# Kernel optimization log

Measured on AMD Instinct MI355X. Metric: run time of the kernel, lower is better.

## Reference

```python
import jax, jax.numpy as jnp
import numpy as np

B, C, H, W = 2, 192, 64, 64
NHEADS = 8


def setup_inputs() -> dict:
    key = jax.random.key(0)
    ks = jax.random.split(key, 6)
    L = H * W
    return {
        "x": jax.random.normal(ks[0], (B, C, H, W), dtype=jnp.float32),
        "mask": jax.random.normal(ks[1], (B, L, L), dtype=jnp.float32),
        "w_qkv": jax.random.normal(ks[2], (3 * C, C), dtype=jnp.float32) * (1.0 / np.sqrt(C)),
        "b_qkv": jax.random.normal(ks[3], (3 * C,), dtype=jnp.float32) * 0.02,
        "w_proj": jax.random.normal(ks[4], (C, C), dtype=jnp.float32) * (1.0 / np.sqrt(C)),
        "b_proj": jax.random.normal(ks[5], (C,), dtype=jnp.float32) * 0.02,
        "num_heads": NHEADS,
    }


def reference(x, mask, w_qkv, b_qkv, w_proj, b_proj, num_heads):
    b, c, h, w = x.shape
    L = h * w
    hd = c // num_heads  # head dim
    # 1x1 conv == per-pixel linear over channels
    qkv = jnp.einsum('bchw,oc->bohw', x, w_qkv) + b_qkv[None, :, None, None]
    q, k, v = jnp.split(qkv, 3, axis=1)  # each [b, c, h, w]

    def to_heads(t):
        # b (head hd) h w -> b head (h w) hd
        return t.reshape(b, num_heads, hd, L).transpose(0, 1, 3, 2)

    q, k, v = to_heads(q), to_heads(k), to_heads(v)
    scale = num_heads ** (-0.5)  # NOTE: original scales by num_heads, not head_dim
    attn = jnp.einsum('bnld,bnmd->bnlm', q, k) * scale + mask[:, None, :, :]
    attn = jax.nn.softmax(attn, axis=-1)
    out = jnp.einsum('bnlm,bnmd->bnld', attn, v)  # [b, head, L, hd]
    # b head L hd -> b (head hd) h w
    out = out.transpose(0, 1, 3, 2).reshape(b, c, h, w)
    out = jnp.einsum('bchw,oc->bohw', out, w_proj) + b_proj[None, :, None, None]
    return out
```

## Files before the change

kernel.cpp:

```cpp
#include <hip/hip_runtime.h>

#define B_  2
#define C_  192
#define L_  4096
#define NH_ 8
#define HD_ 24
#define C3_ 576
#define KV_ 64
#define NSPL_ 4
#define LSPL_ (L_ / NSPL_)
#define NTS_ (LSPL_ / KV_)
#define HG_ 4

typedef _Float16 f16;
typedef __attribute__((ext_vector_type(8))) f16 f16x8;
typedef __attribute__((ext_vector_type(16))) float f32x16;

#define L2E_ 1.4426950408889634f

__device__ __forceinline__ int pk2(float a, float b) {
    union { __fp16 h __attribute__((ext_vector_type(2))); int i; } u;
    u.h = __builtin_amdgcn_cvt_pkrtz(a, b);
    return u.i;
}
__device__ __forceinline__ int pk2_rte(float a, float b) {
    union { f16 h[2]; int i; } u;
    u.h[0] = (f16)a; u.h[1] = (f16)b;
    return u.i;
}
__device__ __forceinline__ float ex2(float x) {
    float r;
    asm("v_exp_f32 %0, %1" : "=v"(r) : "v"(x));
    return r;
}
__device__ __forceinline__ float lg2(float x) {
    float r;
    asm("v_log_f32 %0, %1" : "=v"(r) : "v"(x));
    return r;
}

union Frag { f16x8 v; int i[4]; };

#define MFMA32(A, Bx, Cc) __builtin_amdgcn_mfma_f32_32x32x16_f16((A), (Bx), (Cc), 0, 0, 0)

__device__ __forceinline__ void gload4(const void* g, void* lds) {
    typedef const unsigned int __attribute__((address_space(1))) as1u;
    typedef unsigned int __attribute__((address_space(3))) as3u;
    __builtin_amdgcn_global_load_lds((as1u*)g,
                                     (as3u*)(unsigned int)(unsigned long long)lds,
                                     4, 0, 0);
}
__device__ __forceinline__ void gload16(const void* g, void* lds) {
    typedef const unsigned int __attribute__((address_space(1))) as1u;
    typedef unsigned int __attribute__((address_space(3))) as3u;
    __builtin_amdgcn_global_load_lds((as1u*)g,
                                     (as3u*)(unsigned int)(unsigned long long)lds,
                                     16, 0, 0);
}

__global__ __launch_bounds__(256) void lin_qkv(const float* __restrict__ a,
                                               const float* __restrict__ w,
                                               const float* __restrict__ bias,
                                               unsigned int* __restrict__ q2,
                                               unsigned int* __restrict__ k2,
                                               unsigned short* __restrict__ v16) {
    __shared__ float wl[8][C_];
    const int og  = blockIdx.x;
    const int b   = blockIdx.y >> 4;
    const int lt  = blockIdx.y & 15;
    const int tid = threadIdx.x;

    for (int e = tid; e < 8 * C_; e += 256) wl[e / C_][e % C_] = w[og * 8 * C_ + e];
    __syncthreads();

    const int l = lt * 256 + tid;
    float acc[8];
#pragma unroll
    for (int j = 0; j < 8; ++j) acc[j] = bias[og * 8 + j];

    const float* ap = a + (size_t)b * C_ * L_ + l;
#pragma unroll 2
    for (int c = 0; c < C_; ++c) {
        const float xv = ap[(size_t)c * L_];
#pragma unroll
        for (int j = 0; j < 8; ++j) acc[j] = fmaf(wl[j][c], xv, acc[j]);
    }

    const float qscale = 0.35355339059327373f * L2E_;
    if (og < 48) {
        unsigned int* dst = (og < 24) ? q2 : k2;
        const int og_ = (og < 24) ? og : og - 24;
        const float sc = (og < 24) ? qscale : 1.f;
        const int h = og_ / 3, j0 = (og_ % 3) * 4;
        unsigned int* p = dst + ((size_t)(b * NH_ + h) * 12 + j0) * L_ + l;
#pragma unroll
        for (int j = 0; j < 4; ++j)
            p[(size_t)j * L_] = pk2_rte(acc[2 * j] * sc, acc[2 * j + 1] * sc);
    } else {
        const int og_ = og - 48;
        const int h = og_ / 3, d0 = (og_ % 3) * 8;
        unsigned short* p = v16 + ((size_t)(b * NH_ + h) * 24 + d0) * L_ + l;
#pragma unroll
        for (int j = 0; j < 8; ++j) {
            union { f16 hf; unsigned short us; } cv;
            cv.hf = (f16)acc[j];
            p[(size_t)j * L_] = cv.us;
        }
    }
}

__global__ __launch_bounds__(256) void lin_kernel(const float* __restrict__ a,
                                                  const float* __restrict__ w,
                                                  const float* __restrict__ bias,
                                                  float* __restrict__ out, int OC) {
    __shared__ float wl[8][C_];
    const int og  = blockIdx.x;
    const int b   = blockIdx.y >> 4;
    const int lt  = blockIdx.y & 15;
    const int tid = threadIdx.x;

    for (int e = tid; e < 8 * C_; e += 256) wl[e / C_][e % C_] = w[og * 8 * C_ + e];
    __syncthreads();

    const int l = lt * 256 + tid;
    float acc[8];
#pragma unroll
    for (int j = 0; j < 8; ++j) acc[j] = bias[og * 8 + j];

    const float* ap = a + (size_t)b * C_ * L_ + l;
#pragma unroll 2
    for (int c = 0; c < C_; ++c) {
        const float xv = ap[(size_t)c * L_];
#pragma unroll
        for (int j = 0; j < 8; ++j) acc[j] = fmaf(wl[j][c], xv, acc[j]);
    }

    float* op = out + ((size_t)b * OC + og * 8) * L_ + l;
#pragma unroll
    for (int j = 0; j < 8; ++j) op[(size_t)j * L_] = acc[j];
}

__global__ __launch_bounds__(256) void attn_mfma(const unsigned int* __restrict__ q2,
                                                 const unsigned int* __restrict__ k2,
                                                 const unsigned short* __restrict__ v16,
                                                 const float* __restrict__ mask,
                                                 unsigned short* __restrict__ po,
                                                 float* __restrict__ pms) {
    const int tid  = threadIdx.x;
    const int lane = tid & 63;
    const int wid  = tid >> 6;
    const int hi   = lane >> 5;
    const int lq   = lane & 31;
    const int bid  = blockIdx.x;
    const int qt   = bid & 31;
    const int r    = bid >> 5;
    const int b    = r & 1;
    const int hg   = (r >> 1) & 1;
    const int sp   = r >> 2;
    const int qrow = qt * 128 + wid * 32 + lq;
    const int kv0  = sp * LSPL_;
    const int hbase = hg * HG_;

    __shared__ int k_lds[2][HG_][16][64];
    __shared__ int v_lds[2][HG_][32][32];

#pragma unroll
    for (int z = 0; z < 8; ++z) {
        const int wd = z * 256 + tid;
        k_lds[wd >> 10][(wd >> 8) & 3][12 + ((wd >> 6) & 3)][wd & 63] = 0;
    }

    const unsigned int*   qb   = q2  + (size_t)(b * NH_ + hbase) * 12 * L_;
    const unsigned int*   kb_w = k2  + (size_t)(b * NH_ + hbase + wid) * 12 * L_;
    const unsigned short* vb_w = v16 + (size_t)(b * NH_ + hbase + wid) * 24 * L_;
    const float* mrow = mask + ((size_t)b * L_ + qrow) * L_;

    int bq[HG_][8];
#pragma unroll
    for (int H = 0; H < HG_; ++H)
#pragma unroll
        for (int s = 0; s < 2; ++s)
#pragma unroll
            for (int t = 0; t < 4; ++t) {
                const int dpq = 8 * s + 4 * hi + t;
                bq[H][s * 4 + t] = (dpq < 12) ? qb[(size_t)(H * 12 + dpq) * L_ + qrow] : 0;
            }

#define STAGE(BF, KK) do {                                                    \
    _Pragma("unroll")                                                         \
    for (int j_ = 0; j_ < 3; ++j_) {                                          \
        const int dp_ = j_ * 4 + (lane >> 4);                                 \
        gload16(kb_w + (size_t)dp_ * L_ + (KK) + 4 * (lane & 15),             \
                &k_lds[BF][wid][0][0] + j_ * 256);                            \
    }                                                                         \
    _Pragma("unroll")                                                         \
    for (int j_ = 0; j_ < 12; ++j_) {                                         \
        const int e_ = j_ * 64 + lane;                                        \
        const int d_ = e_ >> 5, sl_ = e_ & 31;                                \
        gload4(vb_w + (size_t)d_ * L_ + (KK) + 2 * (sl_ ^ d_),                \
               &v_lds[BF][wid][0][0] + j_ * 64);                              \
    } } while (0)

#define MLOADX(KK) do {                                                       \
    const float4* mb_ = (const float4*)(mrow + (KK));                         \
    _Pragma("unroll")                                                         \
    for (int q_ = 0; q_ < 4; ++q_) {                                          \
        const float4 t0_ = mb_[2 * q_ + hi];                                  \
        mr0[4 * q_ + 0] = t0_.x; mr0[4 * q_ + 1] = t0_.y;                     \
        mr0[4 * q_ + 2] = t0_.z; mr0[4 * q_ + 3] = t0_.w;                     \
        const float4 t1_ = mb_[8 + 2 * q_ + hi];                              \
        mr1[4 * q_ + 0] = t1_.x; mr1[4 * q_ + 1] = t1_.y;                     \
        mr1[4 * q_ + 2] = t1_.z; mr1[4 * q_ + 3] = t1_.w;                     \
    } } while (0)

#define MSCALE do {                                                           \
    _Pragma("unroll")                                                         \
    for (int i_ = 0; i_ < 16; ++i_) { mr0[i_] *= L2E_; mr1[i_] *= L2E_; }     \
    } while (0)

#define QKH(H, BF) do {                                                       \
    Frag qf0, qf1, ka0, ka1;                                                  \
    _Pragma("unroll")                                                         \
    for (int t_ = 0; t_ < 4; ++t_) { qf0.i[t_] = bq[H][t_]; qf1.i[t_] = bq[H][4 + t_]; } \
    _Pragma("unroll")                                                         \
    for (int t_ = 0; t_ < 4; ++t_) {                                          \
        ka0.i[t_] = k_lds[BF][H][4 * hi + t_][lq];                            \
        ka1.i[t_] = k_lds[BF][H][8 + 4 * hi + t_][lq];                        \
    }                                                                         \
    __builtin_amdgcn_s_setprio(1);                                            \
    c0 = MFMA32(ka0.v, qf0.v, mr0);                                           \
    c0 = MFMA32(ka1.v, qf1.v, c0);                                            \
    __builtin_amdgcn_s_setprio(0);                                            \
    _Pragma("unroll")                                                         \
    for (int t_ = 0; t_ < 4; ++t_) {                                          \
        ka0.i[t_] = k_lds[BF][H][4 * hi + t_][32 + lq];                       \
        ka1.i[t_] = k_lds[BF][H][8 + 4 * hi + t_][32 + lq];                   \
    }                                                                         \
    __builtin_amdgcn_s_setprio(1);                                            \
    c1 = MFMA32(ka0.v, qf0.v, mr1);                                           \
    c1 = MFMA32(ka1.v, qf1.v, c1);                                            \
    __builtin_amdgcn_s_setprio(0);                                            \
    } while (0)

#define PVSTEP(BF, H, CU, U) do {                                             \
    int w1[4], w2[4], s1[4], s2[4];                                           \
    _Pragma("unroll")                                                         \
    for (int q_ = 0; q_ < 4; ++q_) {                                          \
        w1[q_] = pk2(CU[4 * q_], CU[4 * q_ + 1]);                             \
        w2[q_] = pk2(CU[4 * q_ + 2], CU[4 * q_ + 3]);                         \
    }                                                                         \
    _Pragma("unroll")                                                         \
    for (int q_ = 0; q_ < 4; ++q_) {                                          \
        s1[q_] = __shfl_xor(w1[q_], 32);                                      \
        s2[q_] = __shfl_xor(w2[q_], 32);                                      \
    }                                                                         \
    _Pragma("unroll")                                                         \
    for (int s_ = 0; s_ < 2; ++s_) {                                          \
        const int qq_ = 2 * s_ + hi;                                          \
        Frag pb, va;                                                          \
        pb.i[0] = hi ? s1[qq_] : w1[qq_];                                     \
        pb.i[1] = hi ? s2[qq_] : w2[qq_];                                     \
        pb.i[2] = hi ? w1[qq_] : s1[qq_];                                     \
        pb.i[3] = hi ? w2[qq_] : s2[qq_];                                     \
        _Pragma("unroll")                                                     \
        for (int t_ = 0; t_ < 4; ++t_)                                        \
            va.i[t_] = v_lds[BF][H][lq][(16 * U + 8 * s_ + 4 * hi + t_) ^ lq]; \
        __builtin_amdgcn_s_setprio(1);                                        \
        o[H] = MFMA32(va.v, pb.v, o[H]);                                      \
        __builtin_amdgcn_s_setprio(0);                                        \
    } } while (0)

#define SMPV(H, BF) do {                                                      \
    float pmax = c0[0];                                                       \
    _Pragma("unroll")                                                         \
    for (int i_ = 1; i_ < 16; ++i_) pmax = fmaxf(pmax, c0[i_]);               \
    _Pragma("unroll")                                                         \
    for (int i_ = 0; i_ < 16; ++i_) pmax = fmaxf(pmax, c1[i_]);               \
    pmax = fmaxf(pmax, __shfl_xor(pmax, 32));                                 \
    if (!__all((int)(pmax <= mrun[H] + 11.5415603f))) {                       \
        const float newm_ = fmaxf(mrun[H], pmax);                             \
        const float r_ = ex2(mrun[H] - newm_);                                \
        srun[H] *= r_;                                                        \
        _Pragma("unroll")                                                     \
        for (int i_ = 0; i_ < 16; ++i_) o[H][i_] *= r_;                       \
        mrun[H] = newm_;                                                      \
    }                                                                         \
    float ls = 0.f;                                                           \
    _Pragma("unroll")                                                         \
    for (int i_ = 0; i_ < 16; ++i_) { c0[i_] = ex2(c0[i_] - mrun[H]); ls += c0[i_]; } \
    _Pragma("unroll")                                                         \
    for (int i_ = 0; i_ < 16; ++i_) { c1[i_] = ex2(c1[i_] - mrun[H]); ls += c1[i_]; } \
    ls += __shfl_xor(ls, 32);                                                 \
    srun[H] += ls;                                                            \
    PVSTEP(BF, H, c0, 0);                                                     \
    PVSTEP(BF, H, c1, 1);                                                     \
    } while (0)

    f32x16 o[HG_];
    float mrun[HG_], srun[HG_];
#pragma unroll
    for (int H = 0; H < HG_; ++H) {
#pragma unroll
        for (int i = 0; i < 16; ++i) o[H][i] = 0.f;
        mrun[H] = -1e30f;
        srun[H] = 0.f;
    }
    f32x16 mr0, mr1, c0, c1;

    STAGE(0, kv0);
    MLOADX(kv0);
    __syncthreads();

#pragma clang loop unroll(disable)
    for (int t = 0; t < NTS_; ++t) {
        const int kk = kv0 + t * KV_;
        const int cur = t & 1;
        if (t + 1 < NTS_) STAGE(cur ^ 1, kk + KV_);
        MSCALE;
        QKH(0, cur); SMPV(0, cur);
        QKH(1, cur); SMPV(1, cur);
        QKH(2, cur); SMPV(2, cur);
        QKH(3, cur);
        if (t + 1 < NTS_) MLOADX(kk + KV_);
        SMPV(3, cur);
        __syncthreads();
    }

#pragma unroll
    for (int H = 0; H < HG_; ++H) {
        const float inv = 1.f / srun[H];
        const float lse = mrun[H] + lg2(srun[H]);
        unsigned short* pob = po + ((size_t)((sp * B_ + b) * NH_ + hbase + H) * HD_) * L_ + qrow;
#pragma unroll
        for (int i = 0; i < 16; ++i) {
            const int d = (i & 3) + 8 * (i >> 2) + 4 * hi;
            if (d < HD_) {
                union { __fp16 hf; unsigned short us; } cv;
                cv.hf = (__fp16)(o[H][i] * inv);
                pob[(size_t)d * L_] = cv.us;
            }
        }
        if (hi == 0)
            pms[((size_t)(sp * B_ + b) * NH_ + hbase + H) * L_ + qrow] = lse;
    }
#undef STAGE
#undef MLOADX
#undef MSCALE
#undef QKH
#undef PVSTEP
#undef SMPV
}

__global__ __launch_bounds__(256) void combine_kernel(const unsigned short* __restrict__ po,
                                                      const float* __restrict__ pms,
                                                      float* __restrict__ att) {
    const int qrow = blockIdx.x * 256 + threadIdx.x;
    const int h    = blockIdx.y;
    const int b    = blockIdx.z;

    float l[NSPL_];
#pragma unroll
    for (int s = 0; s < NSPL_; ++s)
        l[s] = pms[((size_t)(s * B_ + b) * NH_ + h) * L_ + qrow];
    float lm = l[0];
#pragma unroll
    for (int s = 1; s < NSPL_; ++s) lm = fmaxf(lm, l[s]);
    float wv[NSPL_], wsum = 0.f;
#pragma unroll
    for (int s = 0; s < NSPL_; ++s) { wv[s] = ex2(l[s] - lm); wsum += wv[s]; }
    const float inv = 1.f / wsum;

    float* op = att + ((size_t)b * C_ + h * HD_) * L_ + qrow;
#pragma unroll
    for (int d = 0; d < HD_; ++d) {
        float acc = 0.f;
#pragma unroll
        for (int s = 0; s < NSPL_; ++s) {
            union { unsigned short us; __fp16 hf; } cv;
            cv.us = po[(((size_t)(s * B_ + b) * NH_ + h) * HD_ + d) * L_ + qrow];
            acc += (float)cv.hf * wv[s];
        }
        op[(size_t)d * L_] = acc * inv;
    }
}

extern "C" void kernel_launch(void* const* d_in, const int* in_sizes, int n_in,
                              void* d_out, int out_size, void* d_ws, size_t ws_size,
                              hipStream_t stream) {
    const float* x      = (const float*)d_in[0];
    const float* mask   = (const float*)d_in[1];
    const float* w_qkv  = (const float*)d_in[2];
    const float* b_qkv  = (const float*)d_in[3];
    const float* w_proj = (const float*)d_in[4];
    const float* b_proj = (const float*)d_in[5];
    float* out = (float*)d_out;

    unsigned int*   q2  = (unsigned int*)d_ws;
    unsigned int*   k2  = q2 + (size_t)B_ * NH_ * 12 * L_;
    unsigned short* v16 = (unsigned short*)(k2 + (size_t)B_ * NH_ * 12 * L_);
    unsigned short* po  = v16 + (size_t)B_ * NH_ * HD_ * L_;
    float* pms    = (float*)(po + (size_t)NSPL_ * B_ * NH_ * HD_ * L_);
    float* ws_att = pms + (size_t)NSPL_ * B_ * NH_ * L_;

    lin_qkv<<<dim3(72, 32), 256, 0, stream>>>(x, w_qkv, b_qkv, q2, k2, v16);
    attn_mfma<<<dim3(512), 256, 0, stream>>>(q2, k2, v16, mask, po, pms);
    combine_kernel<<<dim3(16, NH_, B_), 256, 0, stream>>>(po, pms, ws_att);
    lin_kernel<<<dim3(24, 32), 256, 0, stream>>>(ws_att, w_proj, b_proj, out, C_);
}
```

Baseline: 363.7 us.

## Transpose K to key-major padded layout and interleave two heads per softmax stage

K is now written by the QKV projection in a key-major layout padded to 20 words per key, so the attention kernel can stage it with contiguous 16-byte copies and read MFMA fragments as single vector LDS loads. The V swizzle is changed to allow 8-element vector reads. The loop now computes QK for two heads before doing softmax and PV for both, which gives more independent work to hide latency. The lazy-rescale skip is dropped, so the rescale now runs every tile, as are the setprio hints. The padded K buffer uses more workspace and global traffic.

```diff
diff --git a/kernel.cpp b/kernel.cpp
--- a/kernel.cpp
+++ b/kernel.cpp
@@ -11,6 +11,7 @@
 #define LSPL_ (L_ / NSPL_)
 #define NTS_ (LSPL_ / KV_)
 #define HG_ 4
+#define KSTR_ 20
 
 typedef _Float16 f16;
 typedef __attribute__((ext_vector_type(8))) f16 f16x8;
@@ -62,7 +63,7 @@
                                                const float* __restrict__ w,
                                                const float* __restrict__ bias,
                                                unsigned int* __restrict__ q2,
-                                               unsigned int* __restrict__ k2,
+                                               unsigned int* __restrict__ k2t,
                                                unsigned short* __restrict__ v16) {
     __shared__ float wl[8][C_];
     const int og  = blockIdx.x;
@@ -87,15 +88,25 @@
     }
 
     const float qscale = 0.35355339059327373f * L2E_;
-    if (og < 48) {
-        unsigned int* dst = (og < 24) ? q2 : k2;
-        const int og_ = (og < 24) ? og : og - 24;
-        const float sc = (og < 24) ? qscale : 1.f;
+    if (og < 24) {
+        const int h = og / 3, j0 = (og % 3) * 4;
+        unsigned int* p = q2 + ((size_t)(b * NH_ + h) * 12 + j0) * L_ + l;
+#pragma unroll
+        for (int j = 0; j < 4; ++j)
+            p[(size_t)j * L_] = pk2_rte(acc[2 * j] * qscale, acc[2 * j + 1] * qscale);
+    } else if (og < 48) {
+        const int og_ = og - 24;
         const int h = og_ / 3, j0 = (og_ % 3) * 4;
-        unsigned int* p = dst + ((size_t)(b * NH_ + h) * 12 + j0) * L_ + l;
-#pragma unroll
-        for (int j = 0; j < 4; ++j)
-            p[(size_t)j * L_] = pk2_rte(acc[2 * j] * sc, acc[2 * j + 1] * sc);
+        unsigned int* p = k2t + ((size_t)(b * NH_ + h) * L_ + l) * KSTR_ + j0;
+        int4 v;
+        v.x = pk2_rte(acc[0], acc[1]); v.y = pk2_rte(acc[2], acc[3]);
+        v.z = pk2_rte(acc[4], acc[5]); v.w = pk2_rte(acc[6], acc[7]);
+        *(int4*)p = v;
+        if (j0 == 8) {
+            int4 z; z.x = z.y = z.z = z.w = 0;
+            *(int4*)(p + 4) = z;
+            *(int4*)(p + 8) = z;
+        }
     } else {
         const int og_ = og - 48;
         const int h = og_ / 3, d0 = (og_ % 3) * 8;
@@ -141,7 +152,7 @@
 }
 
 __global__ __launch_bounds__(256) void attn_mfma(const unsigned int* __restrict__ q2,
-                                                 const unsigned int* __restrict__ k2,
+                                                 const unsigned int* __restrict__ k2t,
                                                  const unsigned short* __restrict__ v16,
                                                  const float* __restrict__ mask,
                                                  unsigned short* __restrict__ po,
@@ -161,17 +172,11 @@
     const int kv0  = sp * LSPL_;
     const int hbase = hg * HG_;
 
-    __shared__ int k_lds[2][HG_][16][64];
-    __shared__ int v_lds[2][HG_][32][32];
-
-#pragma unroll
-    for (int z = 0; z < 8; ++z) {
-        const int wd = z * 256 + tid;
-        k_lds[wd >> 10][(wd >> 8) & 3][12 + ((wd >> 6) & 3)][wd & 63] = 0;
-    }
+    __shared__ __attribute__((aligned(16))) int k_lds[2][HG_][64 * KSTR_];
+    __shared__ __attribute__((aligned(16))) int v_lds[2][HG_][32 * 32];
 
     const unsigned int*   qb   = q2  + (size_t)(b * NH_ + hbase) * 12 * L_;
-    const unsigned int*   kb_w = k2  + (size_t)(b * NH_ + hbase + wid) * 12 * L_;
+    const unsigned int*   kb_w = k2t + (size_t)(b * NH_ + hbase + wid) * L_ * KSTR_;
     const unsigned short* vb_w = v16 + (size_t)(b * NH_ + hbase + wid) * 24 * L_;
     const float* mrow = mask + ((size_t)b * L_ + qrow) * L_;
 
@@ -187,18 +192,18 @@
             }
 
 #define STAGE(BF, KK) do {                                                    \
-    _Pragma("unroll")                                                         \
-    for (int j_ = 0; j_ < 3; ++j_) {                                          \
-        const int dp_ = j_ * 4 + (lane >> 4);                                 \
-        gload16(kb_w + (size_t)dp_ * L_ + (KK) + 4 * (lane & 15),             \
-                &k_lds[BF][wid][0][0] + j_ * 256);                            \
-    }                                                                         \
+    const char* ksrc_ = (const char*)kb_w + (size_t)(KK) * 80 + (size_t)lane * 16; \
+    char* kdst_ = (char*)&k_lds[BF][wid][0];                                  \
+    _Pragma("unroll")                                                         \
+    for (int j_ = 0; j_ < 5; ++j_)                                            \
+        gload16(ksrc_ + j_ * 1024, kdst_ + j_ * 1024);                        \
     _Pragma("unroll")                                                         \
     for (int j_ = 0; j_ < 12; ++j_) {                                         \
-        const int e_ = j_ * 64 + lane;                                        \
-        const int d_ = e_ >> 5, sl_ = e_ & 31;                                \
-        gload4(vb_w + (size_t)d_ * L_ + (KK) + 2 * (sl_ ^ d_),                \
-               &v_lds[BF][wid][0][0] + j_ * 64);                              \
+        const int d_ = j_ * 2 + (lane >> 5);                                  \
+        const int c_ = lane & 31;                                             \
+        const int kp_ = ((((c_ >> 2) ^ (d_ & 7)) << 2) | (c_ & 3));           \
+        gload4(vb_w + (size_t)d_ * L_ + (KK) + 2 * kp_,                       \
+               (char*)&v_lds[BF][wid][0] + j_ * 256);                         \
     } } while (0)
 
 #define MLOADX(KK) do {                                                       \
@@ -218,83 +223,85 @@
     for (int i_ = 0; i_ < 16; ++i_) { mr0[i_] *= L2E_; mr1[i_] *= L2E_; }     \
     } while (0)
 
-#define QKH(H, BF) do {                                                       \
-    Frag qf0, qf1, ka0, ka1;                                                  \
+#define QKH(BF, H, C0, C1) do {                                               \
+    Frag qf0, qf1, ka;                                                        \
     _Pragma("unroll")                                                         \
     for (int t_ = 0; t_ < 4; ++t_) { qf0.i[t_] = bq[H][t_]; qf1.i[t_] = bq[H][4 + t_]; } \
-    _Pragma("unroll")                                                         \
-    for (int t_ = 0; t_ < 4; ++t_) {                                          \
-        ka0.i[t_] = k_lds[BF][H][4 * hi + t_][lq];                            \
-        ka1.i[t_] = k_lds[BF][H][8 + 4 * hi + t_][lq];                        \
+    const int* kb_ = &k_lds[BF][H][0];                                        \
+    ka.v = *(const f16x8*)(kb_ + lq * KSTR_ + 4 * hi);                        \
+    C0 = MFMA32(ka.v, qf0.v, mr0);                                            \
+    ka.v = *(const f16x8*)(kb_ + lq * KSTR_ + 8 + 4 * hi);                    \
+    C0 = MFMA32(ka.v, qf1.v, C0);                                             \
+    ka.v = *(const f16x8*)(kb_ + (32 + lq) * KSTR_ + 4 * hi);                 \
+    C1 = MFMA32(ka.v, qf0.v, mr1);                                            \
+    ka.v = *(const f16x8*)(kb_ + (32 + lq) * KSTR_ + 8 + 4 * hi);             \
+    C1 = MFMA32(ka.v, qf1.v, C1);                                             \
+    } while (0)
+
+#define SMH(H, C0, C1) do {                                                   \
+    float m8[8], m4[4], m2[2];                                                \
+    _Pragma("unroll")                                                         \
+    for (int i_ = 0; i_ < 8; ++i_)                                            \
+        m8[i_] = fmaxf(fmaxf(C0[i_], C0[i_ + 8]), fmaxf(C1[i_], C1[i_ + 8])); \
+    _Pragma("unroll")                                                         \
+    for (int i_ = 0; i_ < 4; ++i_) m4[i_] = fmaxf(m8[i_], m8[i_ + 4]);        \
+    m2[0] = fmaxf(m4[0], m4[2]); m2[1] = fmaxf(m4[1], m4[3]);                 \
+    float pmax = fmaxf(m2[0], m2[1]);                                         \
+    pmax = fmaxf(pmax, __shfl_xor(pmax, 32));                                 \
+    const float newm_ = fmaxf(mrun[H], pmax);                                 \
+    const float r_ = ex2(mrun[H] - newm_);                                    \
+    mrun[H] = newm_;                                                          \
+    srun[H] *= r_;                                                            \
+    _Pragma("unroll")                                                         \
+    for (int i_ = 0; i_ < 16; ++i_) o[H][i_] *= r_;                           \
+    _Pragma("unroll")                                                         \
+    for (int i_ = 0; i_ < 16; ++i_) C0[i_] = ex2(C0[i_] - newm_);             \
+    _Pragma("unroll")                                                         \
+    for (int i_ = 0; i_ < 16; ++i_) C1[i_] = ex2(C1[i_] - newm_);             \
+    float s8[8], s4[4];                                                       \
+    _Pragma("unroll")                                                         \
+    for (int i_ = 0; i_ < 8; ++i_)                                            \
+        s8[i_] = (C0[i_] + C0[i_ + 8]) + (C1[i_] + C1[i_ + 8]);               \
+    _Pragma("unroll")                                                         \
+    for (int i_ = 0; i_ < 4; ++i_) s4[i_] = s8[i_] + s8[i_ + 4];              \
+    float ls = (s4[0] + s4[2]) + (s4[1] + s4[3]);                             \
+    ls += __shfl_xor(ls, 32);                                                 \
+    srun[H] += ls;                                                            \
+    } while (0)
+
+#define PVH(BF, H, C0, C1) do {                                               \
+    int wa1[4], wa2[4], sa1[4], sa2[4];                                       \
+    int wb1[4], wb2[4], sb1[4], sb2[4];                                       \
+    _Pragma("unroll")                                                         \
+    for (int q_ = 0; q_ < 4; ++q_) {                                          \
+        wa1[q_] = pk2(C0[4 * q_], C0[4 * q_ + 1]);                            \
+        wa2[q_] = pk2(C0[4 * q_ + 2], C0[4 * q_ + 3]);                        \
+        wb1[q_] = pk2(C1[4 * q_], C1[4 * q_ + 1]);                            \
+        wb2[q_] = pk2(C1[4 * q_ + 2], C1[4 * q_ + 3]);                        \
     }                                                                         \
-    __builtin_amdgcn_s_setprio(1);                                            \
-    c0 = MFMA32(ka0.v, qf0.v, mr0);                                           \
-    c0 = MFMA32(ka1.v, qf1.v, c0);                                            \
-    __builtin_amdgcn_s_setprio(0);                                            \
-    _Pragma("unroll")                                                         \
-    for (int t_ = 0; t_ < 4; ++t_) {                                          \
-        ka0.i[t_] = k_lds[BF][H][4 * hi + t_][32 + lq];                       \
-        ka1.i[t_] = k_lds[BF][H][8 + 4 * hi + t_][32 + lq];                   \
+    _Pragma("unroll")                                                         \
+    for (int q_ = 0; q_ < 4; ++q_) {                                          \
+        sa1[q_] = __shfl_xor(wa1[q_], 32); sa2[q_] = __shfl_xor(wa2[q_], 32); \
+        sb1[q_] = __shfl_xor(wb1[q_], 32); sb2[q_] = __shfl_xor(wb2[q_], 32); \
     }                                                                         \
-    __builtin_amdgcn_s_setprio(1);                                            \
-    c1 = MFMA32(ka0.v, qf0.v, mr1);                                           \
-    c1 = MFMA32(ka1.v, qf1.v, c1);                                            \
-    __builtin_amdgcn_s_setprio(0);                                            \
-    } while (0)
-
-#define PVSTEP(BF, H, CU, U) do {                                             \
-    int w1[4], w2[4], s1[4], s2[4];                                           \
-    _Pragma("unroll")                                                         \
-    for (int q_ = 0; q_ < 4; ++q_) {                                          \
-        w1[q_] = pk2(CU[4 * q_], CU[4 * q_ + 1]);                             \
-        w2[q_] = pk2(CU[4 * q_ + 2], CU[4 * q_ + 3]);                         \
-    }                                                                         \
-    _Pragma("unroll")                                                         \
-    for (int q_ = 0; q_ < 4; ++q_) {                                          \
-        s1[q_] = __shfl_xor(w1[q_], 32);                                      \
-        s2[q_] = __shfl_xor(w2[q_], 32);                                      \
-    }                                                                         \
+    const int* vb_ = &v_lds[BF][H][0];                                        \
     _Pragma("unroll")                                                         \
     for (int s_ = 0; s_ < 2; ++s_) {                                          \
         const int qq_ = 2 * s_ + hi;                                          \
         Frag pb, va;                                                          \
-        pb.i[0] = hi ? s1[qq_] : w1[qq_];                                     \
-        pb.i[1] = hi ? s2[qq_] : w2[qq_];                                     \
-        pb.i[2] = hi ? w1[qq_] : s1[qq_];                                     \
-        pb.i[3] = hi ? w2[qq_] : s2[qq_];                                     \
-        _Pragma("unroll")                                                     \
-        for (int t_ = 0; t_ < 4; ++t_)                                        \
-            va.i[t_] = v_lds[BF][H][lq][(16 * U + 8 * s_ + 4 * hi + t_) ^ lq]; \
-        __builtin_amdgcn_s_setprio(1);                                        \
+        pb.i[0] = hi ? sa1[qq_] : wa1[qq_];                                   \
+        pb.i[1] = hi ? sa2[qq_] : wa2[qq_];                                   \
+        pb.i[2] = hi ? wa1[qq_] : sa1[qq_];                                   \
+        pb.i[3] = hi ? wa2[qq_] : sa2[qq_];                                   \
+        va.v = *(const f16x8*)(vb_ + lq * 32 + (((2 * s_ + hi) ^ (lq & 7)) << 2)); \
         o[H] = MFMA32(va.v, pb.v, o[H]);                                      \
-        __builtin_amdgcn_s_setprio(0);                                        \
+        pb.i[0] = hi ? sb1[qq_] : wb1[qq_];                                   \
+        pb.i[1] = hi ? sb2[qq_] : wb2[qq_];                                   \
+        pb.i[2] = hi ? wb1[qq_] : sb1[qq_];                                   \
+        pb.i[3] = hi ? wb2[qq_] : sb2[qq_];                                   \
+        va.v = *(const f16x8*)(vb_ + lq * 32 + (((4 + 2 * s_ + hi) ^ (lq & 7)) << 2)); \
+        o[H] = MFMA32(va.v, pb.v, o[H]);                                      \
     } } while (0)
-
-#define SMPV(H, BF) do {                                                      \
-    float pmax = c0[0];                                                       \
-    _Pragma("unroll")                                                         \
-    for (int i_ = 1; i_ < 16; ++i_) pmax = fmaxf(pmax, c0[i_]);               \
-    _Pragma("unroll")                                                         \
-    for (int i_ = 0; i_ < 16; ++i_) pmax = fmaxf(pmax, c1[i_]);               \
-    pmax = fmaxf(pmax, __shfl_xor(pmax, 32));                                 \
-    if (!__all((int)(pmax <= mrun[H] + 11.5415603f))) {                       \
-        const float newm_ = fmaxf(mrun[H], pmax);                             \
-        const float r_ = ex2(mrun[H] - newm_);                                \
-        srun[H] *= r_;                                                        \
-        _Pragma("unroll")                                                     \
-        for (int i_ = 0; i_ < 16; ++i_) o[H][i_] *= r_;                       \
-        mrun[H] = newm_;                                                      \
-    }                                                                         \
-    float ls = 0.f;                                                           \
-    _Pragma("unroll")                                                         \
-    for (int i_ = 0; i_ < 16; ++i_) { c0[i_] = ex2(c0[i_] - mrun[H]); ls += c0[i_]; } \
-    _Pragma("unroll")                                                         \
-    for (int i_ = 0; i_ < 16; ++i_) { c1[i_] = ex2(c1[i_] - mrun[H]); ls += c1[i_]; } \
-    ls += __shfl_xor(ls, 32);                                                 \
-    srun[H] += ls;                                                            \
-    PVSTEP(BF, H, c0, 0);                                                     \
-    PVSTEP(BF, H, c1, 1);                                                     \
-    } while (0)
 
     f32x16 o[HG_];
     float mrun[HG_], srun[HG_];
@@ -305,7 +312,7 @@
         mrun[H] = -1e30f;
         srun[H] = 0.f;
     }
-    f32x16 mr0, mr1, c0, c1;
+    f32x16 mr0, mr1, cA0, cA1, cB0, cB1;
 
     STAGE(0, kv0);
     MLOADX(kv0);
@@ -317,12 +324,19 @@
         const int cur = t & 1;
         if (t + 1 < NTS_) STAGE(cur ^ 1, kk + KV_);
         MSCALE;
-        QKH(0, cur); SMPV(0, cur);
-        QKH(1, cur); SMPV(1, cur);
-        QKH(2, cur); SMPV(2, cur);
-        QKH(3, cur);
+        QKH(cur, 0, cA0, cA1);
+        QKH(cur, 1, cB0, cB1);
+        SMH(0, cA0, cA1);
+        SMH(1, cB0, cB1);
+        PVH(cur, 0, cA0, cA1);
+        PVH(cur, 1, cB0, cB1);
+        QKH(cur, 2, cA0, cA1);
+        QKH(cur, 3, cB0, cB1);
         if (t + 1 < NTS_) MLOADX(kk + KV_);
-        SMPV(3, cur);
+        SMH(2, cA0, cA1);
+        SMH(3, cB0, cB1);
+        PVH(cur, 2, cA0, cA1);
+        PVH(cur, 3, cB0, cB1);
         __syncthreads();
     }
 
@@ -347,8 +361,8 @@
 #undef MLOADX
 #undef MSCALE
 #undef QKH
-#undef PVSTEP
-#undef SMPV
+#undef SMH
+#undef PVH
 }
 
 __global__ __launch_bounds__(256) void combine_kernel(const unsigned short* __restrict__ po,
@@ -396,14 +410,14 @@
     float* out = (float*)d_out;
 
     unsigned int*   q2  = (unsigned int*)d_ws;
-    unsigned int*   k2  = q2 + (size_t)B_ * NH_ * 12 * L_;
-    unsigned short* v16 = (unsigned short*)(k2 + (size_t)B_ * NH_ * 12 * L_);
+    unsigned int*   k2t = q2 + (size_t)B_ * NH_ * 12 * L_;
+    unsigned short* v16 = (unsigned short*)(k2t + (size_t)B_ * NH_ * L_ * KSTR_);
     unsigned short* po  = v16 + (size_t)B_ * NH_ * HD_ * L_;
     float* pms    = (float*)(po + (size_t)NSPL_ * B_ * NH_ * HD_ * L_);
     float* ws_att = pms + (size_t)NSPL_ * B_ * NH_ * L_;
 
-    lin_qkv<<<dim3(72, 32), 256, 0, stream>>>(x, w_qkv, b_qkv, q2, k2, v16);
-    attn_mfma<<<dim3(512), 256, 0, stream>>>(q2, k2, v16, mask, po, pms);
+    lin_qkv<<<dim3(72, 32), 256, 0, stream>>>(x, w_qkv, b_qkv, q2, k2t, v16);
+    attn_mfma<<<dim3(512), 256, 0, stream>>>(q2, k2t, v16, mask, po, pms);
     combine_kernel<<<dim3(16, NH_, B_), 256, 0, stream>>>(po, pms, ws_att);
     lin_kernel<<<dim3(24, 32), 256, 0, stream>>>(ws_att, w_proj, b_proj, out, C_);
 }
```

After: 354.0 us. -2.7%, faster.
